# Kernel tuning notes

Measured on AMD Instinct MI355X. Metric: run time of the kernel, lower is better.

Reference implementation:

```python
import jax, jax.numpy as jnp
import numpy as np

NH, NKV, HD = 32, 8, 64
ROPE_BASE = 10000.0


def _rope_tables(L, hd):
    inv_freq = 1.0 / (ROPE_BASE ** (jnp.arange(0, hd, 2, dtype=jnp.float32) / hd))
    t = jnp.arange(L, dtype=jnp.float32)
    freqs = jnp.outer(t, inv_freq)              # (L, hd/2)
    emb = jnp.concatenate([freqs, freqs], -1)   # (L, hd)
    return jnp.cos(emb), jnp.sin(emb)


def _rotate_half(x):
    h = x.shape[-1] // 2
    return jnp.concatenate([-x[..., h:], x[..., :h]], axis=-1)


def _apply_rope(x, cos, sin):
    # x: (B, H, L, hd); cos/sin: (L, hd) broadcast over B, H
    return x * cos[None, None] + _rotate_half(x) * sin[None, None]


def setup_inputs() -> dict:
    key = jax.random.key(0)
    ks = jax.random.split(key, 5)
    B, L, H = 2, 2048, 2048
    s = 0.02
    return {
        "x": jax.random.normal(ks[0], (B, L, H), dtype=jnp.float32),
        "wq": jax.random.normal(ks[1], (NH * HD, H), dtype=jnp.float32) * s,
        "wk": jax.random.normal(ks[2], (NKV * HD, H), dtype=jnp.float32) * s,
        "wv": jax.random.normal(ks[3], (NKV * HD, H), dtype=jnp.float32) * s,
        "wo": jax.random.normal(ks[4], (H, NH * HD), dtype=jnp.float32) * s,
    }


def reference(x, wq, wk, wv, wo):
    B, L, H = x.shape
    rep = NH // NKV
    q = (x @ wq.T).reshape(B, L, NH, HD).transpose(0, 2, 1, 3)    # (B, nh, L, hd)
    k = (x @ wk.T).reshape(B, L, NKV, HD).transpose(0, 2, 1, 3)   # (B, nkv, L, hd)
    v = (x @ wv.T).reshape(B, L, NKV, HD).transpose(0, 2, 1, 3)
    cos, sin = _rope_tables(L, HD)
    q = _apply_rope(q, cos, sin)
    k = _apply_rope(k, cos, sin)
    # GQA: group q heads instead of repeating K/V (same math as repeat_interleave)
    qg = q.reshape(B, NKV, rep, L, HD)
    scores = jnp.einsum("bgrqd,bgkd->bgrqk", qg, k) / jnp.sqrt(jnp.float32(HD))
    causal = jnp.tril(jnp.ones((L, L), dtype=bool))
    scores = jnp.where(causal, scores, jnp.float32(-jnp.inf))
    probs = jax.nn.softmax(scores, axis=-1)
    out = jnp.einsum("bgrqk,bgkd->bgrqd", probs, v)               # (B, nkv, rep, L, hd)
    out = out.reshape(B, NH, L, HD).transpose(0, 2, 1, 3).reshape(B, L, NH * HD)
    return out @ wo.T
```

## Files before the change

### kernel.cpp

```cpp
#include <hip/hip_runtime.h>

using u16 = unsigned short;
typedef __attribute__((ext_vector_type(8))) short bf16x8;
typedef __attribute__((ext_vector_type(4))) float f32x4;
typedef __attribute__((ext_vector_type(4))) float float4v;
typedef __attribute__((ext_vector_type(4))) unsigned short us4;

__device__ __forceinline__ u16 f2bf(float f) {
  union { float f; unsigned u; } v; v.f = f;
  unsigned r = v.u + 0x7fffu + ((v.u >> 16) & 1u);
  return (u16)(r >> 16);
}

__device__ __forceinline__ void glds16(const void* g, void* l) {
  __builtin_amdgcn_global_load_lds(
      (const __attribute__((address_space(1))) void*)g,
      (__attribute__((address_space(3))) void*)l, 16, 0, 0);
}

__device__ __forceinline__ void lgkm0() {
  asm volatile("s_waitcnt lgkmcnt(0)" ::: "memory");
}

#define MFMA(a, b, c) __builtin_amdgcn_mfma_f32_16x16x32_bf16((a), (b), (c), 0, 0, 0)

__global__ __launch_bounds__(256) void cvt_bf16(const float* __restrict__ src,
                                                u16* __restrict__ dst, int n4) {
  int i = blockIdx.x * 256 + threadIdx.x;
  if (i >= n4) return;
  float4v v = ((const float4v*)src)[i];
  us4 o;
  o[0] = f2bf(v[0]); o[1] = f2bf(v[1]); o[2] = f2bf(v[2]); o[3] = f2bf(v[3]);
  ((us4*)dst)[i] = o;
}

__global__ __launch_bounds__(256) void rope_tables(float* __restrict__ cos_t,
                                                   float* __restrict__ sin_t) {
  int i = blockIdx.x * 256 + threadIdx.x;
  if (i >= 2048 * 32) return;
  int t = i >> 5, fi = i & 31;
  float inv = powf(10000.f, -(float)fi / 32.f);
  float ang = (float)t * inv;
  cos_t[i] = cosf(ang);
  sin_t[i] = sinf(ang);
}

__global__ __launch_bounds__(256) void gemm_bt(const u16* __restrict__ A,
                                               const u16* __restrict__ B,
                                               float* __restrict__ C,
                                               int M, int N, int K) {
  __shared__ u16 As[128 * 32];
  __shared__ u16 Bs[128 * 32];
  const int tid = threadIdx.x;
  const int w = tid >> 6, l = tid & 63;
  const int wr = w >> 1, wc = w & 1;
  const int lrow = l & 15, lk = (l >> 4) * 8, jr = (l >> 4) * 4;

  f32x4 acc[4][4];
#pragma unroll
  for (int m = 0; m < 4; ++m)
#pragma unroll
    for (int n = 0; n < 4; ++n) acc[m][n] = f32x4{0.f, 0.f, 0.f, 0.f};

  const int st_row = tid >> 2;
  const int st_k = (tid & 3) * 8;
  const u16* a0 = A + (size_t)(blockIdx.x * 128 + st_row) * K + st_k;
  const u16* a1 = a0 + (size_t)64 * K;
  const u16* b0 = B + (size_t)(blockIdx.y * 128 + st_row) * K + st_k;
  const u16* b1 = b0 + (size_t)64 * K;

  u16* Ad0 = &As[w * 512];
  u16* Ad1 = &As[2048 + w * 512];
  u16* Bd0 = &Bs[w * 512];
  u16* Bd1 = &Bs[2048 + w * 512];

  for (int k0 = 0; k0 < K; k0 += 32) {
    glds16(a0, Ad0);
    glds16(a1, Ad1);
    glds16(b0, Bd0);
    glds16(b1, Bd1);
    a0 += 32; a1 += 32; b0 += 32; b1 += 32;
    __syncthreads();
    bf16x8 af[4], bfr[4];
#pragma unroll
    for (int m = 0; m < 4; ++m)
      af[m] = *(const bf16x8*)&As[(wr * 64 + m * 16 + lrow) * 32 + lk];
#pragma unroll
    for (int n = 0; n < 4; ++n)
      bfr[n] = *(const bf16x8*)&Bs[(wc * 64 + n * 16 + lrow) * 32 + lk];
#pragma unroll
    for (int m = 0; m < 4; ++m)
#pragma unroll
      for (int n = 0; n < 4; ++n)
        acc[m][n] = MFMA(af[m], bfr[n], acc[m][n]);
    __syncthreads();
  }

  float* Cp = C + (size_t)(blockIdx.x * 128 + wr * 64) * N + blockIdx.y * 128 + wc * 64;
#pragma unroll
  for (int m = 0; m < 4; ++m)
#pragma unroll
    for (int n = 0; n < 4; ++n)
#pragma unroll
      for (int j = 0; j < 4; ++j)
        Cp[(size_t)(m * 16 + jr + j) * N + n * 16 + lrow] = acc[m][n][j];
}

__global__ __launch_bounds__(256) void rope_apply(
    const float* __restrict__ qkv, const float* __restrict__ cos_t,
    const float* __restrict__ sin_t, u16* __restrict__ q_r,
    u16* __restrict__ k_r, u16* __restrict__ v_t) {
  int idx = blockIdx.x * 256 + threadIdx.x;
  if (idx >= 2 * 2048 * 3072) return;
  int c = idx % 3072;
  int bl = idx / 3072;
  int l = bl & 2047, b = bl >> 11;
  float val = qkv[idx];
  if (c < 2048) {
    int h = c >> 6, d = c & 63;
    float cs = cos_t[l * 32 + (d & 31)];
    float sn = sin_t[l * 32 + (d & 31)];
    float other = qkv[(size_t)bl * 3072 + h * 64 + ((d < 32) ? d + 32 : d - 32)];
    float r = (d < 32) ? (val * cs - other * sn) : (val * cs + other * sn);
    q_r[(((size_t)b * 32 + h) * 2048 + l) * 64 + d] = f2bf(r);
  } else if (c < 2560) {
    int cc = c - 2048, h = cc >> 6, d = cc & 63;
    float cs = cos_t[l * 32 + (d & 31)];
    float sn = sin_t[l * 32 + (d & 31)];
    float other = qkv[(size_t)bl * 3072 + 2048 + h * 64 + ((d < 32) ? d + 32 : d - 32)];
    float r = (d < 32) ? (val * cs - other * sn) : (val * cs + other * sn);
    k_r[(((size_t)b * 8 + h) * 2048 + l) * 64 + d] = f2bf(r);
  } else {
    int cc = c - 2560, h = cc >> 6, d = cc & 63;
    v_t[(((size_t)b * 8 + h) * 64 + d) * 2048 + l] = f2bf(val);
  }
}

__global__ __launch_bounds__(256) void attn2(const u16* __restrict__ q_r,
                                             const u16* __restrict__ k_r,
                                             const u16* __restrict__ v_t,
                                             u16* __restrict__ attn_o) {
  __shared__ u16 Kl[2][64 * 64];
  __shared__ u16 Vl[2][64 * 64];
  __shared__ u16 Pl[4][32 * 64];
  __shared__ float Al[4][2][16];

  const int bid = blockIdx.x;
  const int q0 = (63 - (bid >> 4)) * 32;
  const int bk = bid & 15;
  const int b = bk >> 3, kvh = bk & 7;

  const int tid = threadIdx.x;
  const int w = tid >> 6;
  const int l = tid & 63;
  const int h = kvh * 4 + w;
  const int lr = l & 15, lg = l >> 4;

  const u16* Qp = q_r + (((size_t)(b * 32 + h)) * 2048 + q0) * 64;
  const u16* Kp = k_r + ((size_t)(b * 8 + kvh)) * 2048 * 64;
  const u16* Vp = v_t + ((size_t)(b * 8 + kvh)) * 64 * 2048;

  bf16x8 qf[2][2];
#pragma unroll
  for (int qh = 0; qh < 2; ++qh)
#pragma unroll
    for (int kh = 0; kh < 2; ++kh)
      qf[qh][kh] = *(const bf16x8*)&Qp[(qh * 16 + lr) * 64 + kh * 32 + lg * 8];

  f32x4 o[2][4];
#pragma unroll
  for (int qh = 0; qh < 2; ++qh)
#pragma unroll
    for (int nf = 0; nf < 4; ++nf) o[qh][nf] = f32x4{0.f, 0.f, 0.f, 0.f};
  float m[2] = {-1e30f, -1e30f}, ls[2] = {0.f, 0.f};

  const int sr = l >> 3;
  const int sc = (l & 7) ^ sr;
  const int nt = (q0 + 95) >> 6;

  auto stage = [&](int bufi, int t) {
#pragma unroll
    for (int p = 0; p < 2; ++p) {
      const int r = p * 32 + w * 8 + sr;
      glds16(Kp + (size_t)(t * 64 + r) * 64 + sc * 8, &Kl[bufi][(p * 32 + w * 8) * 64]);
      glds16(Vp + (size_t)r * 2048 + t * 64 + sc * 8, &Vl[bufi][(p * 32 + w * 8) * 64]);
    }
  };

  stage(0, 0);
  int buf = 0;
  for (int t = 0; t < nt; ++t) {
    __syncthreads();
    if (t + 1 < nt) stage(buf ^ 1, t + 1);
    const int kv0 = t * 64;

    f32x4 s[2][4];
#pragma unroll
    for (int qh = 0; qh < 2; ++qh)
#pragma unroll
      for (int kv4 = 0; kv4 < 4; ++kv4) s[qh][kv4] = f32x4{0.f, 0.f, 0.f, 0.f};
    const int swz = (lr & 7) << 4;
#pragma unroll
    for (int kv4 = 0; kv4 < 4; ++kv4) {
      const int kvr = kv4 * 16 + lr;
#pragma unroll
      for (int kh = 0; kh < 2; ++kh) {
        bf16x8 kf = *(const bf16x8*)((const char*)&Kl[buf][kvr * 64] +
                                     ((kh * 64 + lg * 16) ^ swz));
        s[0][kv4] = MFMA(kf, qf[0][kh], s[0][kv4]);
        s[1][kv4] = MFMA(kf, qf[1][kh], s[1][kv4]);
      }
    }

    const bool full = (kv0 + 63 <= q0);
#pragma unroll
    for (int qh = 0; qh < 2; ++qh) {
      const int qrow = q0 + qh * 16 + lr;
      float pm = -1e30f;
#pragma unroll
      for (int kv4 = 0; kv4 < 4; ++kv4)
#pragma unroll
        for (int j = 0; j < 4; ++j) {
          float v = s[qh][kv4][j] * 0.125f;
          if (!full && (kv0 + kv4 * 16 + lg * 4 + j) > qrow) v = -1e30f;
          s[qh][kv4][j] = v;
          pm = fmaxf(pm, v);
        }
      pm = fmaxf(pm, __shfl_xor(pm, 16));
      pm = fmaxf(pm, __shfl_xor(pm, 32));
      if (!__all(pm <= m[qh])) {
        const float mn = fmaxf(m[qh], pm);
        const float al = __expf(m[qh] - mn);
        m[qh] = mn;
        ls[qh] *= al;
        Al[w][qh][lr] = al;
        lgkm0();
        const f32x4 a4 = *(const f32x4*)&Al[w][qh][lg * 4];
#pragma unroll
        for (int nf = 0; nf < 4; ++nf)
#pragma unroll
          for (int j = 0; j < 4; ++j) o[qh][nf][j] *= a4[j];
      }
      float rs = 0.f;
#pragma unroll
      for (int kv4 = 0; kv4 < 4; ++kv4) {
        us4 pk;
#pragma unroll
        for (int j = 0; j < 4; ++j) {
          const float p = __expf(s[qh][kv4][j] - m[qh]);
          rs += p;
          pk[j] = f2bf(p);
        }
        *(us4*)((char*)&Pl[w][(qh * 16 + lr) * 64] +
                ((kv4 * 32 + lg * 8) ^ swz)) = pk;
      }
      rs += __shfl_xor(rs, 16);
      rs += __shfl_xor(rs, 32);
      ls[qh] += rs;
    }

    lgkm0();
#pragma unroll
    for (int k2 = 0; k2 < 2; ++k2) {
      bf16x8 pa[2];
#pragma unroll
      for (int qh = 0; qh < 2; ++qh)
        pa[qh] = *(const bf16x8*)((const char*)&Pl[w][(qh * 16 + lr) * 64] +
                                  ((k2 * 64 + lg * 16) ^ swz));
#pragma unroll
      for (int nf = 0; nf < 4; ++nf) {
        const int d = nf * 16 + lr;
        bf16x8 bv = *(const bf16x8*)((const char*)&Vl[buf][d * 64] +
                                     ((k2 * 64 + lg * 16) ^ swz));
        o[0][nf] = MFMA(pa[0], bv, o[0][nf]);
        o[1][nf] = MFMA(pa[1], bv, o[1][nf]);
      }
    }
    buf ^= 1;
  }

  Al[w][0][lr] = ls[0];
  Al[w][1][lr] = ls[1];
  lgkm0();
  u16* Op = attn_o + (size_t)b * 2048 * 2048 + h * 64;
#pragma unroll
  for (int qh = 0; qh < 2; ++qh) {
    const f32x4 l4 = *(const f32x4*)&Al[w][qh][lg * 4];
#pragma unroll
    for (int j = 0; j < 4; ++j) {
      const float inv = __builtin_amdgcn_rcpf(l4[j]);
      const int row = q0 + qh * 16 + lg * 4 + j;
#pragma unroll
      for (int nf = 0; nf < 4; ++nf)
        Op[(size_t)row * 2048 + nf * 16 + lr] = f2bf(o[qh][nf][j] * inv);
    }
  }
}

extern "C" void kernel_launch(void* const* d_in, const int* in_sizes, int n_in,
                              void* d_out, int out_size, void* d_ws, size_t ws_size,
                              hipStream_t stream) {
  const float* x = (const float*)d_in[0];
  const float* wq = (const float*)d_in[1];
  const float* wk = (const float*)d_in[2];
  const float* wv = (const float*)d_in[3];
  const float* wo = (const float*)d_in[4];
  float* out = (float*)d_out;

  char* p = (char*)d_ws;
  auto alloc = [&](size_t bytes) {
    char* r = p;
    p += (bytes + 255) & ~(size_t)255;
    return r;
  };
  u16* x_bf   = (u16*)alloc((size_t)8388608 * 2);
  u16* wqkv   = (u16*)alloc((size_t)3072 * 2048 * 2);
  u16* wo_bf  = (u16*)alloc((size_t)2048 * 2048 * 2);
  float* qkv  = (float*)alloc((size_t)4096 * 3072 * 4);
  u16* q_r    = (u16*)alloc((size_t)8388608 * 2);
  u16* k_r    = (u16*)alloc((size_t)2097152 * 2);
  u16* v_t    = (u16*)alloc((size_t)2097152 * 2);
  u16* attn_o = (u16*)alloc((size_t)8388608 * 2);
  float* cos_t = (float*)alloc((size_t)65536 * 4);
  float* sin_t = (float*)alloc((size_t)65536 * 4);

  cvt_bf16<<<8192, 256, 0, stream>>>(x, x_bf, 2097152);
  cvt_bf16<<<4096, 256, 0, stream>>>(wq, wqkv, 1048576);
  cvt_bf16<<<1024, 256, 0, stream>>>(wk, wqkv + (size_t)2048 * 2048, 262144);
  cvt_bf16<<<1024, 256, 0, stream>>>(wv, wqkv + (size_t)2560 * 2048, 262144);
  cvt_bf16<<<4096, 256, 0, stream>>>(wo, wo_bf, 1048576);
  rope_tables<<<256, 256, 0, stream>>>(cos_t, sin_t);

  gemm_bt<<<dim3(32, 24), 256, 0, stream>>>(x_bf, wqkv, qkv, 4096, 3072, 2048);

  rope_apply<<<49152, 256, 0, stream>>>(qkv, cos_t, sin_t, q_r, k_r, v_t);

  attn2<<<1024, 256, 0, stream>>>(q_r, k_r, v_t, attn_o);

  gemm_bt<<<dim3(32, 16), 256, 0, stream>>>(attn_o, wo_bf, out, 4096, 2048, 2048);
}
```

Measured before the change: 372.7 us.

## Fuse RoPE and Q/K/V layout epilogue into QKV GEMM, fold softmax scale into Q

The QKV projection GEMM now applies RoPE in its epilogue and writes bf16 Q, K and transposed V directly. This removes the fp32 qkv intermediate and the separate rope_apply pass over roughly 50MB. The softmax scale and log2(e) are folded into Q so attention can use exp2f without a per-score multiply, and masking now runs only on diagonal tiles. Cos and sin are packed into a single float2 table. The epilogue stores are scattered 2-byte writes, which may be less efficient than the old coalesced layout.

```diff
diff --git a/kernel.cpp b/kernel.cpp
--- a/kernel.cpp
+++ b/kernel.cpp
@@ -23,6 +23,8 @@
 }
 
 #define MFMA(a, b, c) __builtin_amdgcn_mfma_f32_16x16x32_bf16((a), (b), (c), 0, 0, 0)
+
+#define QSCALE 0.1803368801111601f
 
 __global__ __launch_bounds__(256) void cvt_bf16(const float* __restrict__ src,
                                                 u16* __restrict__ dst, int n4) {
@@ -34,15 +36,13 @@
   ((us4*)dst)[i] = o;
 }
 
-__global__ __launch_bounds__(256) void rope_tables(float* __restrict__ cos_t,
-                                                   float* __restrict__ sin_t) {
+__global__ __launch_bounds__(256) void rope_cs(float2* __restrict__ cs) {
   int i = blockIdx.x * 256 + threadIdx.x;
   if (i >= 2048 * 32) return;
   int t = i >> 5, fi = i & 31;
   float inv = powf(10000.f, -(float)fi / 32.f);
   float ang = (float)t * inv;
-  cos_t[i] = cosf(ang);
-  sin_t[i] = sinf(ang);
+  cs[i] = make_float2(cosf(ang), sinf(ang));
 }
 
 __global__ __launch_bounds__(256) void gemm_bt(const u16* __restrict__ A,
@@ -106,37 +106,108 @@
         Cp[(size_t)(m * 16 + jr + j) * N + n * 16 + lrow] = acc[m][n][j];
 }
 
-__global__ __launch_bounds__(256) void rope_apply(
-    const float* __restrict__ qkv, const float* __restrict__ cos_t,
-    const float* __restrict__ sin_t, u16* __restrict__ q_r,
-    u16* __restrict__ k_r, u16* __restrict__ v_t) {
-  int idx = blockIdx.x * 256 + threadIdx.x;
-  if (idx >= 2 * 2048 * 3072) return;
-  int c = idx % 3072;
-  int bl = idx / 3072;
-  int l = bl & 2047, b = bl >> 11;
-  float val = qkv[idx];
-  if (c < 2048) {
-    int h = c >> 6, d = c & 63;
-    float cs = cos_t[l * 32 + (d & 31)];
-    float sn = sin_t[l * 32 + (d & 31)];
-    float other = qkv[(size_t)bl * 3072 + h * 64 + ((d < 32) ? d + 32 : d - 32)];
-    float r = (d < 32) ? (val * cs - other * sn) : (val * cs + other * sn);
-    q_r[(((size_t)b * 32 + h) * 2048 + l) * 64 + d] = f2bf(r);
-  } else if (c < 2560) {
-    int cc = c - 2048, h = cc >> 6, d = cc & 63;
-    float cs = cos_t[l * 32 + (d & 31)];
-    float sn = sin_t[l * 32 + (d & 31)];
-    float other = qkv[(size_t)bl * 3072 + 2048 + h * 64 + ((d < 32) ? d + 32 : d - 32)];
-    float r = (d < 32) ? (val * cs - other * sn) : (val * cs + other * sn);
-    k_r[(((size_t)b * 8 + h) * 2048 + l) * 64 + d] = f2bf(r);
+__global__ __launch_bounds__(256) void gemm_qkv(const u16* __restrict__ A,
+                                                const u16* __restrict__ B,
+                                                const float2* __restrict__ cs,
+                                                u16* __restrict__ q_r,
+                                                u16* __restrict__ k_r,
+                                                u16* __restrict__ v_t) {
+  const int K = 2048;
+  __shared__ u16 As[128 * 32];
+  __shared__ u16 Bs[128 * 32];
+  const int tid = threadIdx.x;
+  const int w = tid >> 6, l = tid & 63;
+  const int wr = w >> 1, wc = w & 1;
+  const int lrow = l & 15, lk = (l >> 4) * 8, jr = (l >> 4) * 4;
+
+  f32x4 acc[4][4];
+#pragma unroll
+  for (int m = 0; m < 4; ++m)
+#pragma unroll
+    for (int n = 0; n < 4; ++n) acc[m][n] = f32x4{0.f, 0.f, 0.f, 0.f};
+
+  const int st_row = tid >> 2;
+  const int st_k = (tid & 3) * 8;
+  const u16* a0 = A + (size_t)(blockIdx.x * 128 + st_row) * K + st_k;
+  const u16* a1 = a0 + (size_t)64 * K;
+  const u16* b0 = B + (size_t)(blockIdx.y * 128 + st_row) * K + st_k;
+  const u16* b1 = b0 + (size_t)64 * K;
+
+  u16* Ad0 = &As[w * 512];
+  u16* Ad1 = &As[2048 + w * 512];
+  u16* Bd0 = &Bs[w * 512];
+  u16* Bd1 = &Bs[2048 + w * 512];
+
+  for (int k0 = 0; k0 < K; k0 += 32) {
+    glds16(a0, Ad0);
+    glds16(a1, Ad1);
+    glds16(b0, Bd0);
+    glds16(b1, Bd1);
+    a0 += 32; a1 += 32; b0 += 32; b1 += 32;
+    __syncthreads();
+    bf16x8 af[4], bfr[4];
+#pragma unroll
+    for (int m = 0; m < 4; ++m)
+      af[m] = *(const bf16x8*)&As[(wr * 64 + m * 16 + lrow) * 32 + lk];
+#pragma unroll
+    for (int n = 0; n < 4; ++n)
+      bfr[n] = *(const bf16x8*)&Bs[(wc * 64 + n * 16 + lrow) * 32 + lk];
+#pragma unroll
+    for (int m = 0; m < 4; ++m)
+#pragma unroll
+      for (int n = 0; n < 4; ++n)
+        acc[m][n] = MFMA(af[m], bfr[n], acc[m][n]);
+    __syncthreads();
+  }
+
+  const int cb = blockIdx.y * 128 + wc * 64;
+  const int rowbase = blockIdx.x * 128 + wr * 64;
+
+  if (cb < 2560) {
+    const bool isQ = (cb < 2048);
+    const int h = (isQ ? cb : cb - 2048) >> 6;
+    u16* dst = isQ ? q_r : k_r;
+    const int nh = isQ ? 32 : 8;
+#pragma unroll
+    for (int m = 0; m < 4; ++m) {
+#pragma unroll
+      for (int j = 0; j < 4; ++j) {
+        const int row = rowbase + m * 16 + jr + j;
+        const int b = row >> 11, ll = row & 2047;
+        const float2 c0 = cs[ll * 32 + lrow];
+        const float2 c1 = cs[ll * 32 + 16 + lrow];
+        u16* op = dst + (((size_t)b * nh + h) * 2048 + ll) * 64;
+#pragma unroll
+        for (int n = 0; n < 4; ++n) {
+          const float val = acc[m][n][j];
+          const float oth = acc[m][n ^ 2][j];
+          const float cx = (n & 1) ? c1.x : c0.x;
+          const float sy = (n & 1) ? c1.y : c0.y;
+          float r = (n < 2) ? (val * cx - oth * sy) : (val * cx + oth * sy);
+          if (isQ) r *= QSCALE;
+          op[n * 16 + lrow] = f2bf(r);
+        }
+      }
+    }
   } else {
-    int cc = c - 2560, h = cc >> 6, d = cc & 63;
-    v_t[(((size_t)b * 8 + h) * 64 + d) * 2048 + l] = f2bf(val);
+    const int h = (cb - 2560) >> 6;
+#pragma unroll
+    for (int m = 0; m < 4; ++m) {
+      const int row0 = rowbase + m * 16 + jr;
+      const int b = row0 >> 11, l0 = row0 & 2047;
+#pragma unroll
+      for (int n = 0; n < 4; ++n) {
+        const int d = n * 16 + lrow;
+        us4 pk;
+#pragma unroll
+        for (int j = 0; j < 4; ++j) pk[j] = f2bf(acc[m][n][j]);
+        *(us4*)&v_t[(((size_t)b * 8 + h) * 64 + d) * 2048 + l0] = pk;
+      }
+    }
   }
 }
 
-__global__ __launch_bounds__(256) void attn2(const u16* __restrict__ q_r,
+__global__ __launch_bounds__(256) void attn3(const u16* __restrict__ q_r,
                                              const u16* __restrict__ k_r,
                                              const u16* __restrict__ v_t,
                                              u16* __restrict__ attn_o) {
@@ -177,6 +248,7 @@
   const int sr = l >> 3;
   const int sc = (l & 7) ^ sr;
   const int nt = (q0 + 95) >> 6;
+  const int nfull = q0 >> 6;
 
   auto stage = [&](int bufi, int t) {
 #pragma unroll
@@ -212,25 +284,27 @@
       }
     }
 
-    const bool full = (kv0 + 63 <= q0);
+    const bool diag = (t >= nfull);
 #pragma unroll
     for (int qh = 0; qh < 2; ++qh) {
       const int qrow = q0 + qh * 16 + lr;
+      if (diag) {
+#pragma unroll
+        for (int kv4 = 0; kv4 < 4; ++kv4)
+#pragma unroll
+          for (int j = 0; j < 4; ++j)
+            if ((kv0 + kv4 * 16 + lg * 4 + j) > qrow) s[qh][kv4][j] = -1e30f;
+      }
       float pm = -1e30f;
 #pragma unroll
       for (int kv4 = 0; kv4 < 4; ++kv4)
 #pragma unroll
-        for (int j = 0; j < 4; ++j) {
-          float v = s[qh][kv4][j] * 0.125f;
-          if (!full && (kv0 + kv4 * 16 + lg * 4 + j) > qrow) v = -1e30f;
-          s[qh][kv4][j] = v;
-          pm = fmaxf(pm, v);
-        }
+        for (int j = 0; j < 4; ++j) pm = fmaxf(pm, s[qh][kv4][j]);
       pm = fmaxf(pm, __shfl_xor(pm, 16));
       pm = fmaxf(pm, __shfl_xor(pm, 32));
       if (!__all(pm <= m[qh])) {
         const float mn = fmaxf(m[qh], pm);
-        const float al = __expf(m[qh] - mn);
+        const float al = exp2f(m[qh] - mn);
         m[qh] = mn;
         ls[qh] *= al;
         Al[w][qh][lr] = al;
@@ -247,7 +321,7 @@
         us4 pk;
 #pragma unroll
         for (int j = 0; j < 4; ++j) {
-          const float p = __expf(s[qh][kv4][j] - m[qh]);
+          const float p = exp2f(s[qh][kv4][j] - m[qh]);
           rs += p;
           pk[j] = f2bf(p);
         }
@@ -313,29 +387,25 @@
     p += (bytes + 255) & ~(size_t)255;
     return r;
   };
-  u16* x_bf   = (u16*)alloc((size_t)8388608 * 2);
-  u16* wqkv   = (u16*)alloc((size_t)3072 * 2048 * 2);
-  u16* wo_bf  = (u16*)alloc((size_t)2048 * 2048 * 2);
-  float* qkv  = (float*)alloc((size_t)4096 * 3072 * 4);
-  u16* q_r    = (u16*)alloc((size_t)8388608 * 2);
-  u16* k_r    = (u16*)alloc((size_t)2097152 * 2);
-  u16* v_t    = (u16*)alloc((size_t)2097152 * 2);
-  u16* attn_o = (u16*)alloc((size_t)8388608 * 2);
-  float* cos_t = (float*)alloc((size_t)65536 * 4);
-  float* sin_t = (float*)alloc((size_t)65536 * 4);
+  u16* x_bf    = (u16*)alloc((size_t)8388608 * 2);
+  u16* wqkv    = (u16*)alloc((size_t)3072 * 2048 * 2);
+  u16* wo_bf   = (u16*)alloc((size_t)2048 * 2048 * 2);
+  u16* q_r     = (u16*)alloc((size_t)8388608 * 2);
+  u16* k_r     = (u16*)alloc((size_t)2097152 * 2);
+  u16* v_t     = (u16*)alloc((size_t)2097152 * 2);
+  u16* attn_o  = (u16*)alloc((size_t)8388608 * 2);
+  float2* cs   = (float2*)alloc((size_t)65536 * 8);
 
   cvt_bf16<<<8192, 256, 0, stream>>>(x, x_bf, 2097152);
   cvt_bf16<<<4096, 256, 0, stream>>>(wq, wqkv, 1048576);
   cvt_bf16<<<1024, 256, 0, stream>>>(wk, wqkv + (size_t)2048 * 2048, 262144);
   cvt_bf16<<<1024, 256, 0, stream>>>(wv, wqkv + (size_t)2560 * 2048, 262144);
   cvt_bf16<<<4096, 256, 0, stream>>>(wo, wo_bf, 1048576);
-  rope_tables<<<256, 256, 0, stream>>>(cos_t, sin_t);
-
-  gemm_bt<<<dim3(32, 24), 256, 0, stream>>>(x_bf, wqkv, qkv, 4096, 3072, 2048);
-
-  rope_apply<<<49152, 256, 0, stream>>>(qkv, cos_t, sin_t, q_r, k_r, v_t);
-
-  attn2<<<1024, 256, 0, stream>>>(q_r, k_r, v_t, attn_o);
+  rope_cs<<<256, 256, 0, stream>>>(cs);
+
+  gemm_qkv<<<dim3(32, 24), 256, 0, stream>>>(x_bf, wqkv, cs, q_r, k_r, v_t);
+
+  attn3<<<1024, 256, 0, stream>>>(q_r, k_r, v_t, attn_o);
 
   gemm_bt<<<dim3(32, 16), 256, 0, stream>>>(attn_o, wo_bf, out, 4096, 2048, 2048);
 }
```

Result: faster. 358.7 us (-3.8%).
